# Kernel optimization log

Hardware: AMD Instinct MI355X
Metric: run time of the kernel (lower is better)

The kernel has to match this reference:

```python
import jax, jax.numpy as jnp
import numpy as np

N_HEAD, D_HEAD, D_MODEL, D_INNER, KSIZE = 16, 64, 1024, 4096, 3
LN_EPS = 1e-3  # keras LayerNormalization default epsilon


def _layernorm(x, g, b):
    m = jnp.mean(x, axis=-1, keepdims=True)
    v = jnp.var(x, axis=-1, keepdims=True)
    return (x - m) * jax.lax.rsqrt(v + LN_EPS) * g + b


def _conv1d_same(x, w, b):
    # x: [B, S, Cin], w: [K, Cin, Cout] (keras Conv1D layout)
    y = jax.lax.conv_general_dilated(x, w, window_strides=(1,), padding='SAME',
                                     dimension_numbers=('NWC', 'WIO', 'NWC'))
    return y + b


def setup_inputs() -> dict:
    key = jax.random.key(0)
    ks = jax.random.split(key, 12)
    B, S, D = 4, 1024, D_MODEL
    dec_inp = jax.random.normal(ks[0], (B, S, D), dtype=jnp.float32)
    # padding mask: True = valid token; ensure >=1 padded position per row
    lengths = jax.random.randint(ks[1], (B,), S // 2, S)
    mask = (jnp.arange(S)[None, :] < lengths[:, None])[:, :, None]  # [B,S,1] bool
    sd = 0.02
    qkv_w = jax.random.normal(ks[2], (D, 3 * N_HEAD * D_HEAD), dtype=jnp.float32) * sd
    qkv_b = jnp.zeros((3 * N_HEAD * D_HEAD,), dtype=jnp.float32)
    o_w = jax.random.normal(ks[3], (N_HEAD * D_HEAD, D), dtype=jnp.float32) * sd
    ln1_g = jnp.ones((D,), dtype=jnp.float32)
    ln1_b = jnp.zeros((D,), dtype=jnp.float32)
    conv1_w = jax.random.normal(ks[4], (KSIZE, D, D_INNER), dtype=jnp.float32) * sd
    conv1_b = jnp.zeros((D_INNER,), dtype=jnp.float32)
    conv2_w = jax.random.normal(ks[5], (KSIZE, D_INNER, D), dtype=jnp.float32) * sd
    conv2_b = jnp.zeros((D,), dtype=jnp.float32)
    ln2_g = jnp.ones((D,), dtype=jnp.float32)
    ln2_b = jnp.zeros((D,), dtype=jnp.float32)
    return dict(dec_inp=dec_inp, mask=mask, qkv_w=qkv_w, qkv_b=qkv_b, o_w=o_w,
                ln1_g=ln1_g, ln1_b=ln1_b, conv1_w=conv1_w, conv1_b=conv1_b,
                conv2_w=conv2_w, conv2_b=conv2_b, ln2_g=ln2_g, ln2_b=ln2_b)


def _forward(dec_inp, mask, qkv_w, qkv_b, o_w, ln1_g, ln1_b,
             conv1_w, conv1_b, conv2_w, conv2_b, ln2_g, ln2_b):
    B, S, D = dec_inp.shape
    H, dh = N_HEAD, D_HEAD
    scale = 1.0 / (dh ** 0.5)
    # --- MultiHeadAttn (post-lnorm; dropout inactive at inference) ---
    residual = dec_inp
    qkv = dec_inp @ qkv_w + qkv_b                       # [B,S,3*H*dh]
    hq, hk, hv = jnp.split(qkv, 3, axis=2)
    to_flat = lambda h: h.reshape(B, S, H, dh).transpose(0, 2, 1, 3).reshape(B * H, S, dh)
    q, k, v = to_flat(hq), to_flat(hk), to_flat(hv)
    score = jnp.einsum('bqd,bkd->bqk', q, k) * scale    # [B*H, S, S]
    # attn_mask = ~mask.squeeze(2): True at PAD positions (faithful to TF port)
    am = (~mask[:, :, 0]).astype(score.dtype)[:, None, :]    # [B,1,S]
    am = jnp.tile(am, (H, S, 1))                             # [B*H,S,S] (tile over batch axis, as in tf.tile)
    add = jnp.where(am.astype(bool), am, -jnp.inf)           # pad -> +1.0, valid -> -inf (as written in source)
    score = score + add
    prob = jax.nn.softmax(score, axis=2)
    vec = prob @ v                                      # [B*H,S,dh]
    # faithful to source reshapes: [B*H,S,dh] -> [H,B,S,dh] -> [B,S,H*dh]
    vec = vec.reshape(H, B, S, dh).transpose(1, 2, 0, 3).reshape(B, S, H * dh)
    attn_out = vec @ o_w
    out = _layernorm(residual + attn_out, ln1_g, ln1_b)
    # mask-multiply between blocks
    out = out * mask.astype(out.dtype)
    # --- PositionwiseConvFF (post-lnorm) ---
    core = _conv1d_same(out, conv1_w, conv1_b)
    core = jax.nn.relu(core)
    core = _conv1d_same(core, conv2_w, conv2_b)
    out = _layernorm(out + core, ln2_g, ln2_b)
    out = out * mask.astype(out.dtype)
    return out


def reference(dec_inp, mask, qkv_w, qkv_b, o_w, ln1_g, ln1_b,
              conv1_w, conv1_b, conv2_w, conv2_b, ln2_g, ln2_b):
    return _forward(dec_inp, mask, qkv_w, qkv_b, o_w, ln1_g, ln1_b,
                    conv1_w, conv1_b, conv2_w, conv2_b, ln2_g, ln2_b)
```

## Files before the change

### kernel.cpp

```cpp
#include <hip/hip_runtime.h>
#include <cstdint>
#include <cstddef>

typedef float f32x4 __attribute__((ext_vector_type(4)));
typedef __bf16 bf16x8 __attribute__((ext_vector_type(8)));
typedef unsigned short u16;

__device__ __forceinline__ float bf2f(u16 u) {
  union { unsigned int i; float f; } x; x.i = ((unsigned int)u) << 16; return x.f;
}
__device__ __forceinline__ u16 f2bf(float f) {
  union { float f; unsigned int i; } x; x.f = f;
  unsigned int i = x.i;
  i += 0x7fffu + ((i >> 16) & 1u);
  return (u16)(i >> 16);
}

#if defined(__has_builtin)
#if __has_builtin(__builtin_amdgcn_global_load_lds)
#define HAS_GLL 1
#endif
#endif

__device__ __forceinline__ void async16(const u16* g, u16* l) {
#ifdef HAS_GLL
  __builtin_amdgcn_global_load_lds((const __attribute__((address_space(1))) void*)(const void*)g,
                                   (__attribute__((address_space(3))) void*)(void*)l, 16, 0, 0);
#else
  *(uint4*)l = *(const uint4*)g;
#endif
}

__global__ void compact_mask(const unsigned char* __restrict__ mask,
                             int* __restrict__ padIdx, int* __restrict__ padCnt,
                             float* __restrict__ maskf) {
  const int b = blockIdx.x;
  const int lane = threadIdx.x;
  int stride = 1;
  if (mask[1] == 0) stride = (mask[4] != 0) ? 4 : 8;
  int cnt = 0;
  for (int s0 = 0; s0 < 1024; s0 += 64) {
    const int s = s0 + lane;
    const bool valid = (mask[(size_t)((b << 10) + s) * stride] != 0);
    maskf[(b << 10) + s] = valid ? 1.f : 0.f;
    const bool pad = !valid;
    const unsigned long long bal = __ballot(pad);
    const int rank = (int)__popcll(bal & ((1ull << lane) - 1ull));
    if (pad) padIdx[(b << 10) + cnt + rank] = s;
    cnt += (int)__popcll(bal);
  }
  if (lane == 0) padCnt[b] = cnt;
}

__global__ __launch_bounds__(256)
void f32_to_bf16(const float* __restrict__ in, u16* __restrict__ out, int n4) {
  const int i = blockIdx.x * 256 + threadIdx.x;
  if (i < n4) {
    const float4 v = ((const float4*)in)[i];
    u16 o[4] = { f2bf(v.x), f2bf(v.y), f2bf(v.z), f2bf(v.w) };
    ((ushort4*)out)[i] = *(const ushort4*)o;
  }
}

__global__ __launch_bounds__(256)
void transpose_f32_bf16(const float* __restrict__ in, u16* __restrict__ out, int R, int C) {
  __shared__ u16 tile[64][65];
  const int r0 = blockIdx.y << 6, c0 = blockIdx.x << 6;
  const int tid = threadIdx.x;
  const int lr = tid >> 3, lc = (tid & 7) << 3;
#pragma unroll
  for (int p = 0; p < 2; ++p) {
    const int row = lr + (p << 5);
    const float4 a = *(const float4*)(in + (size_t)(r0 + row) * C + c0 + lc);
    const float4 bq = *(const float4*)(in + (size_t)(r0 + row) * C + c0 + lc + 4);
    tile[row][lc + 0] = f2bf(a.x); tile[row][lc + 1] = f2bf(a.y);
    tile[row][lc + 2] = f2bf(a.z); tile[row][lc + 3] = f2bf(a.w);
    tile[row][lc + 4] = f2bf(bq.x); tile[row][lc + 5] = f2bf(bq.y);
    tile[row][lc + 6] = f2bf(bq.z); tile[row][lc + 7] = f2bf(bq.w);
  }
  __syncthreads();
#pragma unroll
  for (int p = 0; p < 2; ++p) {
    const int oc = lr + (p << 5);
    u16 tmp[8];
#pragma unroll
    for (int e = 0; e < 8; ++e) tmp[e] = tile[lc + e][oc];
    *(uint4*)(out + (size_t)(c0 + oc) * R + r0 + lc) = *(const uint4*)tmp;
  }
}

template<int NTAPS, bool RELU, int SPLITK, int KORIG, int NBN>
__global__ __launch_bounds__(256)
void gemm_bt(const u16* __restrict__ A, const u16* __restrict__ BT,
             const float* __restrict__ bias, u16* __restrict__ C, u16* __restrict__ Calt,
             int M, int N, const u16* __restrict__ zp) {
  __shared__ __align__(16) u16 As[128 * 64];
  __shared__ __align__(16) u16 Bs[128 * 64];
  const int tid = threadIdx.x;
  const int id = blockIdx.x + NBN * blockIdx.y;
  const int bm = ((id / (16 * NBN)) << 4) + (id & 15);
  const int bn = (id % (16 * NBN)) >> 4;
  const int m0 = bm << 7;
  const int n0 = bn << 7;
  const int kz = (SPLITK > 1) ? blockIdx.z : 0;
  constexpr int Ktot = NTAPS * KORIG;
  constexpr int kchunk = Ktot / SPLITK;
  const int lane = tid & 63;
  const int w = tid >> 6;
  const int wm = (w >> 1) << 6;
  const int wn = (w & 1) << 6;
  const int fr = lane & 15;
  const int quad = lane >> 4;
  const int srow = tid >> 3;
  const int scol = (tid & 7) << 3;
  const int sx = (((tid & 7) ^ (srow & 7)) << 3);

  f32x4 acc[4][4] = {};

  const int kbeg = kz * kchunk, kend = kbeg + kchunk;
  int k = kbeg;
  while (k < kend) {
    const int t = (NTAPS == 3) ? (k / KORIG) : 0;
    const int seg_end = (NTAPS == 3) ? min(kend, (t + 1) * KORIG) : kend;
    const int c0 = k - t * KORIG;
    const u16* aptr[4];
    const u16* bptr[4];
#pragma unroll
    for (int i = 0; i < 4; ++i) {
      const int row = srow + (i << 5);
      if (NTAPS == 3) {
        const int m = m0 + row;
        const int sp = (m & 1023) + t - 1;
        aptr[i] = ((unsigned)sp < 1024u) ? (A + (size_t)(m + t - 1) * KORIG + c0 + sx)
                                         : (zp + ((tid & 255) << 3));
      } else {
        aptr[i] = A + (size_t)(m0 + row) * KORIG + k + sx;
      }
      bptr[i] = BT + (size_t)(n0 + row) * Ktot + k + sx;
    }
    for (; k < seg_end; k += 64) {
#pragma unroll
      for (int i = 0; i < 4; ++i) {
        const int row = srow + (i << 5);
        async16(aptr[i], &As[(row << 6) + scol]);
        async16(bptr[i], &Bs[(row << 6) + scol]);
        aptr[i] += 64; bptr[i] += 64;
      }
      asm volatile("s_waitcnt vmcnt(0)" ::: "memory");
      __syncthreads();
#pragma unroll
      for (int ks = 0; ks < 64; ks += 32) {
        const int ccol = ((((ks >> 3) + quad) ^ (fr & 7)) << 3);
        bf16x8 af[4], bfr[4];
#pragma unroll
        for (int mi = 0; mi < 4; ++mi)
          af[mi] = *(const bf16x8*)&As[((wm + (mi << 4) + fr) << 6) + ccol];
#pragma unroll
        for (int ni = 0; ni < 4; ++ni)
          bfr[ni] = *(const bf16x8*)&Bs[((wn + (ni << 4) + fr) << 6) + ccol];
#pragma unroll
        for (int mi = 0; mi < 4; ++mi)
#pragma unroll
          for (int ni = 0; ni < 4; ++ni)
            acc[mi][ni] = __builtin_amdgcn_mfma_f32_16x16x32_bf16(af[mi], bfr[ni], acc[mi][ni], 0, 0, 0);
      }
      __syncthreads();
    }
  }
  const int rbase = m0 + wm + (quad << 2);
  const int cbase = n0 + wn + fr;
  u16* dst = C;
  if (SPLITK > 1 && kz > 0) dst = Calt + (size_t)(kz - 1) * ((size_t)M * N);
#pragma unroll
  for (int ni = 0; ni < 4; ++ni) {
    const int col = cbase + (ni << 4);
    const float bv = (SPLITK == 1 && bias) ? bias[col] : 0.f;
#pragma unroll
    for (int mi = 0; mi < 4; ++mi) {
#pragma unroll
      for (int r = 0; r < 4; ++r) {
        float v = acc[mi][ni][r] + bv;
        if (RELU) v = fmaxf(v, 0.f);
        dst[(size_t)(rbase + (mi << 4) + r) * N + col] = f2bf(v);
      }
    }
  }
}

__global__ __launch_bounds__(256)
void gather_v(const u16* __restrict__ qkv, const int* __restrict__ padIdx,
              const int* __restrict__ padCnt, u16* __restrict__ Vt) {
  const int bm = blockIdx.x;
  const int jt = blockIdx.y;
  const int b = bm >> 2, mb = bm & 3;
  const int npad = padCnt[mb];
  const int npadR = (npad + 63) & ~63;
  if (jt * 64 >= npadR) return;
  const int tid = threadIdx.x;
  __shared__ int rows[64];
  if (tid < 64) {
    const int j = jt * 64 + tid;
    const int jj = j < npad ? j : npad - 1;
    rows[tid] = padIdx[(mb << 10) + jj];
  }
  __shared__ u16 tile[64][72];
  for (int c = 0; c < 16; ++c) {
    const int ch0 = c << 6;
    __syncthreads();
#pragma unroll
    for (int p = 0; p < 2; ++p) {
      const int r = (tid >> 3) + (p << 5);
      const int ch = (tid & 7) << 3;
      const uint4 v = *(const uint4*)(qkv + (size_t)((b << 10) + rows[r]) * 3072 + 2048 + ch0 + ch);
      const u16* us = (const u16*)&v;
#pragma unroll
      for (int e = 0; e < 8; ++e) tile[r][ch + e] = us[e];
    }
    __syncthreads();
#pragma unroll
    for (int p = 0; p < 2; ++p) {
      const int r = (tid >> 3) + (p << 5);
      const int jc = (tid & 7) << 3;
      u16 tmp[8];
#pragma unroll
      for (int e = 0; e < 8; ++e) tmp[e] = tile[jc + e][r];
      *(uint4*)(Vt + (size_t)((bm << 10) + ch0 + r) * 512 + jt * 64 + jc) = *(const uint4*)tmp;
    }
  }
}

__global__ __launch_bounds__(256)
void attn_mfma(const u16* __restrict__ qkv, const u16* __restrict__ Vt,
               const int* __restrict__ padIdx, const int* __restrict__ padCnt,
               u16* __restrict__ vecS) {
  __shared__ __align__(16) u16 Ks[64 * 64];
  __shared__ __align__(16) u16 Vts[64 * 64];
  __shared__ __align__(16) u16 Ps[4][32 * 88];
  __shared__ int rowsIdx[512];
  const int i = blockIdx.x;
  const int qt = blockIdx.y;
  const int b = i >> 4, h = i & 15;
  const int mb = h & 3, bm = (b << 2) + mb;
  const int h_out = i >> 2;
  const int npad = padCnt[mb];
  const int nkt = (npad + 63) >> 6;
  const int tid = threadIdx.x;
  const int w = tid >> 6, lane = tid & 63;
  const int fr = lane & 15, quad = lane >> 4, fko = quad << 3;
  const int srow = tid >> 3, scol = (tid & 7) << 3;
  const int sx = (((tid & 7) ^ (srow & 7)) << 3);

#pragma unroll
  for (int p = 0; p < 2; ++p) {
    const int j = (p << 8) + tid;
    const int jj = j < npad ? j : npad - 1;
    rowsIdx[j] = padIdx[(mb << 10) + jj];
  }

  const int qw = (qt << 7) + (w << 5);
  bf16x8 qf[2][2];
#pragma unroll
  for (int rt = 0; rt < 2; ++rt)
#pragma unroll
    for (int ks = 0; ks < 2; ++ks)
      qf[rt][ks] = *(const bf16x8*)(qkv + (size_t)((b << 10) + qw + (rt << 4) + fr) * 3072 +
                                    (h << 6) + (ks << 5) + fko);

  f32x4 O[2][4];
  float mrun[2][4], lrun[2][4];
#pragma unroll
  for (int rt = 0; rt < 2; ++rt)
#pragma unroll
    for (int r = 0; r < 4; ++r) {
      mrun[rt][r] = -1e30f; lrun[rt][r] = 0.f;
#pragma unroll
      for (int dt = 0; dt < 4; ++dt) O[rt][dt][r] = 0.f;
    }
  __syncthreads();

  for (int kt = 0; kt < nkt; ++kt) {
#pragma unroll
    for (int p = 0; p < 2; ++p) {
      const int r = srow + (p << 5);
      const int grow = rowsIdx[(kt << 6) + r];
      async16(qkv + (size_t)((b << 10) + grow) * 3072 + 1024 + (h << 6) + sx,
              &Ks[(r << 6) + scol]);
      async16(Vt + (size_t)((bm << 10) + (h << 6) + r) * 512 + (kt << 6) + sx,
              &Vts[(r << 6) + scol]);
    }
    asm volatile("s_waitcnt vmcnt(0)" ::: "memory");
    __syncthreads();

    f32x4 S[2][4];
#pragma unroll
    for (int rt = 0; rt < 2; ++rt)
#pragma unroll
      for (int nt = 0; nt < 4; ++nt)
#pragma unroll
        for (int r = 0; r < 4; ++r) S[rt][nt][r] = 0.f;
#pragma unroll
    for (int ks = 0; ks < 2; ++ks) {
      const int ccol = ((((ks << 2) + quad) ^ (fr & 7)) << 3);
      bf16x8 bfr[4];
#pragma unroll
      for (int nt = 0; nt < 4; ++nt)
        bfr[nt] = *(const bf16x8*)&Ks[(((nt << 4) + fr) << 6) + ccol];
#pragma unroll
      for (int rt = 0; rt < 2; ++rt)
#pragma unroll
        for (int nt = 0; nt < 4; ++nt)
          S[rt][nt] = __builtin_amdgcn_mfma_f32_16x16x32_bf16(qf[rt][ks], bfr[nt], S[rt][nt], 0, 0, 0);
    }

#pragma unroll
    for (int nt = 0; nt < 4; ++nt) {
      const int key = (kt << 6) + (nt << 4) + fr;
      const bool dead = (key >= npad);
#pragma unroll
      for (int rt = 0; rt < 2; ++rt)
#pragma unroll
        for (int r = 0; r < 4; ++r) {
          float s = S[rt][nt][r] * 0.125f;
          S[rt][nt][r] = dead ? -1e30f : s;
        }
    }

#pragma unroll
    for (int rt = 0; rt < 2; ++rt) {
#pragma unroll
      for (int r = 0; r < 4; ++r) {
        float mx = fmaxf(fmaxf(S[rt][0][r], S[rt][1][r]), fmaxf(S[rt][2][r], S[rt][3][r]));
#pragma unroll
        for (int off = 1; off <= 8; off <<= 1) mx = fmaxf(mx, __shfl_xor(mx, off, 64));
        const float mnew = fmaxf(mrun[rt][r], mx);
        const float alpha = __expf(mrun[rt][r] - mnew);
        mrun[rt][r] = mnew;
        float rsum = 0.f;
#pragma unroll
        for (int nt = 0; nt < 4; ++nt) {
          const float p_ = __expf(S[rt][nt][r] - mnew);
          S[rt][nt][r] = p_;
          rsum += p_;
        }
#pragma unroll
        for (int off = 1; off <= 8; off <<= 1) rsum += __shfl_xor(rsum, off, 64);
        lrun[rt][r] = lrun[rt][r] * alpha + rsum;
#pragma unroll
        for (int dt = 0; dt < 4; ++dt) O[rt][dt][r] *= alpha;
      }
    }

    u16* ps = &Ps[w][0];
#pragma unroll
    for (int rt = 0; rt < 2; ++rt)
#pragma unroll
      for (int nt = 0; nt < 4; ++nt)
#pragma unroll
        for (int r = 0; r < 4; ++r)
          ps[((rt << 4) + (quad << 2) + r) * 88 + (nt << 4) + fr] = f2bf(S[rt][nt][r]);
    asm volatile("s_waitcnt lgkmcnt(0)" ::: "memory");

#pragma unroll
    for (int ks = 0; ks < 2; ++ks) {
      const int ccol = ((((ks << 2) + quad) ^ (fr & 7)) << 3);
      bf16x8 af[2], bv[4];
#pragma unroll
      for (int rt = 0; rt < 2; ++rt)
        af[rt] = *(const bf16x8*)&ps[((rt << 4) + fr) * 88 + (ks << 5) + fko];
#pragma unroll
      for (int dt = 0; dt < 4; ++dt)
        bv[dt] = *(const bf16x8*)&Vts[(((dt << 4) + fr) << 6) + ccol];
#pragma unroll
      for (int rt = 0; rt < 2; ++rt)
#pragma unroll
        for (int dt = 0; dt < 4; ++dt)
          O[rt][dt] = __builtin_amdgcn_mfma_f32_16x16x32_bf16(af[rt], bv[dt], O[rt][dt], 0, 0, 0);
    }
    __syncthreads();
  }

#pragma unroll
  for (int rt = 0; rt < 2; ++rt)
#pragma unroll
    for (int r = 0; r < 4; ++r) {
      const float inv = 1.f / lrun[rt][r];
      const int q = qw + (rt << 4) + (quad << 2) + r;
      u16* orow = vecS + (size_t)((mb << 10) + q) * 1024 + (h_out << 6);
#pragma unroll
      for (int dt = 0; dt < 4; ++dt)
        orow[(dt << 4) + fr] = f2bf(O[rt][dt][r] * inv);
    }
}

template<bool XF32, bool OUTF32, bool HASB>
__global__ __launch_bounds__(256)
void ln_red4(const void* __restrict__ Xv, const u16* __restrict__ P0,
             const u16* __restrict__ P1, int MN,
             const float* __restrict__ bias,
             const float* __restrict__ g, const float* __restrict__ be,
             const float* __restrict__ maskf, void* __restrict__ outv) {
  const int r = blockIdx.x;
  const int tid = threadIdx.x;
  const size_t base = (size_t)r << 10;
  const float* Xf = (const float*)Xv;
  const u16* Xb = (const u16*)Xv;
  float x[4];
  float s1 = 0.f, s2 = 0.f;
#pragma unroll
  for (int j = 0; j < 4; ++j) {
    const int c = (tid << 2) + j;
    const size_t idx = base + c;
    float y = bf2f(P0[idx]) + bf2f(P1[idx]) + bf2f(P1[MN + idx]) + bf2f(P1[2 * (size_t)MN + idx]);
    if (HASB) y += bias[c];
    const float xv = XF32 ? Xf[idx] : bf2f(Xb[idx]);
    const float v = xv + y;
    x[j] = v; s1 += v; s2 += v * v;
  }
#pragma unroll
  for (int off = 32; off > 0; off >>= 1) { s1 += __shfl_xor(s1, off, 64); s2 += __shfl_xor(s2, off, 64); }
  __shared__ float rs1[4], rs2[4];
  if ((tid & 63) == 0) { rs1[tid >> 6] = s1; rs2[tid >> 6] = s2; }
  __syncthreads();
  s1 = rs1[0] + rs1[1] + rs1[2] + rs1[3];
  s2 = rs2[0] + rs2[1] + rs2[2] + rs2[3];
  const float mean = s1 * (1.f / 1024.f);
  const float var = s2 * (1.f / 1024.f) - mean * mean;
  const float rstd = rsqrtf(var + 1e-3f);
  const float mv = maskf[r];
#pragma unroll
  for (int j = 0; j < 4; ++j) {
    const int c = (tid << 2) + j;
    const float y = ((x[j] - mean) * rstd * g[c] + be[c]) * mv;
    if (OUTF32) ((float*)outv)[base + c] = y;
    else ((u16*)outv)[base + c] = f2bf(y);
  }
}

extern "C" void kernel_launch(void* const* d_in, const int* in_sizes, int n_in,
                              void* d_out, int out_size, void* d_ws, size_t ws_size,
                              hipStream_t stream) {
  (void)in_sizes; (void)n_in; (void)out_size; (void)ws_size;
  const float* dec  = (const float*)d_in[0];
  const unsigned char* mask = (const unsigned char*)d_in[1];
  const float* wqkv = (const float*)d_in[2];
  const float* bqkv = (const float*)d_in[3];
  const float* wo   = (const float*)d_in[4];
  const float* g1   = (const float*)d_in[5];
  const float* b1   = (const float*)d_in[6];
  const float* w1   = (const float*)d_in[7];
  const float* bc1  = (const float*)d_in[8];
  const float* w2   = (const float*)d_in[9];
  const float* bc2  = (const float*)d_in[10];
  const float* g2   = (const float*)d_in[11];
  const float* b2   = (const float*)d_in[12];
  char* ws = (char*)d_ws;
  u16*   zp    = (u16*)(ws + 0);
  int*   pcnt  = (int*)(ws + 16384);
  float* maskf = (float*)(ws + 20480);
  int*   pidx  = (int*)(ws + 40960);
  u16*   decB  = (u16*)(ws + 65536);
  u16*   wqkvT = (u16*)(ws + 8454144);
  u16*   woT   = (u16*)(ws + 14745600);
  u16*   w1T   = (u16*)(ws + 16842752);
  u16*   w2T   = (u16*)(ws + 42008576);
  u16*   qkv   = (u16*)(ws + 67174400);
  u16*   Vt    = (u16*)(ws + 92340224);
  u16*   vecS  = (u16*)(ws + 109117440);
  u16*   x1bf  = (u16*)(ws + 8454144);
  u16*   ybuf  = (u16*)(ws + 67174400);
  u16*   aP0   = (u16*)(ws + 65536);
  u16*   aP1   = (u16*)(ws + 67174400);
  u16*   cP0   = (u16*)(ws + 65536);
  u16*   cP1   = (u16*)(ws + 16842752);

  hipMemsetAsync(zp, 0, 16384, stream);
  compact_mask<<<dim3(4), dim3(64), 0, stream>>>(mask, pidx, pcnt, maskf);
  f32_to_bf16<<<dim3(4096), dim3(256), 0, stream>>>(dec, decB, 1048576);
  transpose_f32_bf16<<<dim3(48, 16), dim3(256), 0, stream>>>(wqkv, wqkvT, 1024, 3072);
  transpose_f32_bf16<<<dim3(16, 16), dim3(256), 0, stream>>>(wo, woT, 1024, 1024);
  transpose_f32_bf16<<<dim3(64, 48), dim3(256), 0, stream>>>(w1, w1T, 3072, 4096);
  transpose_f32_bf16<<<dim3(16, 192), dim3(256), 0, stream>>>(w2, w2T, 12288, 1024);
  gemm_bt<1, false, 1, 1024, 24><<<dim3(24, 32), dim3(256), 0, stream>>>(decB, wqkvT, bqkv, qkv, nullptr, 4096, 3072, zp);
  gather_v<<<dim3(16, 8), dim3(256), 0, stream>>>(qkv, pidx, pcnt, Vt);
  attn_mfma<<<dim3(64, 8), dim3(256), 0, stream>>>(qkv, Vt, pidx, pcnt, vecS);
  gemm_bt<1, false, 4, 1024, 8><<<dim3(8, 32, 4), dim3(256), 0, stream>>>(vecS, woT, nullptr, aP0, aP1, 4096, 1024, zp);
  ln_red4<true, false, false><<<dim3(4096), dim3(256), 0, stream>>>(dec, aP0, aP1, 4194304, nullptr, g1, b1, maskf, x1bf);
  gemm_bt<3, true, 1, 1024, 32><<<dim3(32, 32), dim3(256), 0, stream>>>(x1bf, w1T, bc1, ybuf, nullptr, 4096, 4096, zp);
  gemm_bt<3, false, 4, 4096, 8><<<dim3(8, 32, 4), dim3(256), 0, stream>>>(ybuf, w2T, nullptr, cP0, cP1, 4096, 1024, zp);
  ln_red4<false, true, true><<<dim3(4096), dim3(256), 0, stream>>>(x1bf, cP0, cP1, 4194304, bc2, g2, b2, maskf, (float*)d_out);
}
```

Baseline: 556.2 us.

## Add 256x256 eight-wave GEMM with phased pipelining for QKV and conv FF

Adds a new GEMM kernel with 512 threads and 256x256 output tiles. Each tile is split into four 128-row/col quadrants, staged asynchronously into LDS, and interleaved with MFMA phases under setprio and fine-grained barriers. The QKV projection and both conv1d FF GEMMs now use this kernel instead of the 128-tile gemm_bt, aiming for more data reuse per LDS load and better overlap of loads with compute. The trade-offs are fewer blocks (192-256 per launch) on a large CU count, higher register and LDS use, and reliance on hand-counted vmcnt waits.

```diff
diff --git a/kernel.cpp b/kernel.cpp
--- a/kernel.cpp
+++ b/kernel.cpp
@@ -185,6 +185,142 @@
       }
     }
   }
+}
+
+#define BAR8() do { asm volatile("" ::: "memory"); __builtin_amdgcn_s_barrier(); asm volatile("" ::: "memory"); } while (0)
+#define WAITV(N) asm volatile("s_waitcnt vmcnt(" #N ")" ::: "memory")
+
+#define READ_A(SLOT) \
+  _Pragma("unroll") for (int mi = 0; mi < 4; ++mi) \
+  _Pragma("unroll") for (int ks = 0; ks < 2; ++ks) \
+    af[mi][ks] = *(const bf16x8*)&As[SLOT][((wm + (mi << 4) + fr) << 6) + ((((ks << 2) + quad) ^ (fr & 7)) << 3)];
+#define READ_B(SLOT, BFR) \
+  _Pragma("unroll") for (int ni = 0; ni < 2; ++ni) \
+  _Pragma("unroll") for (int ks = 0; ks < 2; ++ks) \
+    BFR[ni][ks] = *(const bf16x8*)&Bs[SLOT][((wn + (ni << 4) + fr) << 6) + ((((ks << 2) + quad) ^ (fr & 7)) << 3)];
+#define MFMA_PH(MH, NH, BFR) \
+  __builtin_amdgcn_s_setprio(1); \
+  _Pragma("unroll") for (int mi = 0; mi < 4; ++mi) \
+  _Pragma("unroll") for (int ni = 0; ni < 2; ++ni) \
+  _Pragma("unroll") for (int ks = 0; ks < 2; ++ks) \
+    acc[MH][mi][NH][ni] = __builtin_amdgcn_mfma_f32_16x16x32_bf16(af[mi][ks], BFR[ni][ks], acc[MH][mi][NH][ni], 0, 0, 0); \
+  __builtin_amdgcn_s_setprio(0)
+
+template<int NTAPS, bool RELU, int SPLITK, int KORIG>
+__global__ __launch_bounds__(512, 2)
+void gemm8(const u16* __restrict__ A, const u16* __restrict__ BT,
+           const float* __restrict__ bias, u16* __restrict__ C, u16* __restrict__ Calt,
+           int M, int N, const u16* __restrict__ zp) {
+  __shared__ __align__(16) u16 As[4][128 * 64];
+  __shared__ __align__(16) u16 Bs[4][128 * 64];
+  constexpr int Ktot = NTAPS * KORIG;
+  constexpr int kchunk = Ktot / SPLITK;
+  constexpr int NT = kchunk / 64;
+  const int tid = threadIdx.x;
+  const int id = blockIdx.x;
+  const int bm = id & 15, bn = id >> 4;
+  const int m0 = bm << 8, n0 = bn << 8;
+  const int kz = (SPLITK > 1) ? blockIdx.z : 0;
+  const int kbeg = kz * kchunk;
+  const int lane = tid & 63, w = tid >> 6;
+  const int wm = (w >> 2) << 6;
+  const int wn = (w & 3) << 5;
+  const int fr = lane & 15, quad = lane >> 4;
+  const int srow = tid >> 3;
+  const int scol = (tid & 7) << 3;
+  const int sx = (((tid & 7) ^ (srow & 7)) << 3);
+
+  const u16* bp[2][2];
+#pragma unroll
+  for (int nh = 0; nh < 2; ++nh)
+#pragma unroll
+    for (int j = 0; j < 2; ++j)
+      bp[nh][j] = BT + (size_t)(n0 + (nh << 7) + srow + (j << 6)) * Ktot + kbeg + sx;
+
+  auto stageA = [&](int ts, int mh) {
+    const int k = kbeg + (ts << 6);
+    const int tap = (NTAPS == 3) ? (k / KORIG) : 0;
+    const int c0 = k - tap * KORIG;
+    u16* dst = &As[((ts & 1) << 1) | mh][(srow << 6) + scol];
+    const int mrow = m0 + (mh << 7) + srow;
+#pragma unroll
+    for (int j = 0; j < 2; ++j) {
+      const int m = mrow + (j << 6);
+      const u16* src;
+      if (NTAPS == 1) {
+        src = A + (size_t)m * KORIG + c0 + sx;
+      } else {
+        const int sp = (m & 1023) + tap - 1;
+        src = ((unsigned)sp < 1024u) ? (A + (size_t)(m + tap - 1) * KORIG + c0 + sx)
+                                     : (zp + ((tid & 255) << 3));
+      }
+      async16(src, dst + (j << 12));
+    }
+  };
+  auto stageB = [&](int ts, int nh) {
+    u16* dst = &Bs[((ts & 1) << 1) | nh][(srow << 6) + scol];
+#pragma unroll
+    for (int j = 0; j < 2; ++j) {
+      async16(bp[nh][j], dst + (j << 12));
+      bp[nh][j] += 64;
+    }
+  };
+
+  f32x4 acc[2][4][2][2] = {};
+  bf16x8 af[4][2], bf0[2][2], bf1[2][2];
+
+  stageA(0, 0); stageB(0, 0); stageB(0, 1); stageA(0, 1);
+  WAITV(4);
+  BAR8();
+
+#pragma unroll 2
+  for (int t = 0; t < NT; ++t) {
+    const int s0 = (t & 1) << 1, s1 = s0 | 1;
+    const bool pf = (t + 1 < NT);
+    if (pf) stageA(t + 1, 0);
+    READ_A(s0);
+    READ_B(s0, bf0);
+    BAR8();
+    MFMA_PH(0, 0, bf0);
+    if (pf) { WAITV(4); } else { WAITV(2); }
+    BAR8();
+    if (pf) stageB(t + 1, 0);
+    READ_B(s1, bf1);
+    BAR8();
+    MFMA_PH(0, 1, bf1);
+    if (pf) { WAITV(4); } else { WAITV(0); }
+    BAR8();
+    if (pf) stageB(t + 1, 1);
+    READ_A(s1);
+    BAR8();
+    MFMA_PH(1, 1, bf1);
+    BAR8();
+    if (pf) stageA(t + 1, 1);
+    BAR8();
+    MFMA_PH(1, 0, bf0);
+    if (pf) { WAITV(4); }
+    BAR8();
+  }
+
+  u16* dst = C;
+  if (SPLITK > 1 && kz > 0) dst = Calt + (size_t)(kz - 1) * ((size_t)M * N);
+#pragma unroll
+  for (int mh = 0; mh < 2; ++mh)
+#pragma unroll
+    for (int nh = 0; nh < 2; ++nh)
+#pragma unroll
+      for (int ni = 0; ni < 2; ++ni) {
+        const int col = n0 + (nh << 7) + wn + (ni << 4) + fr;
+        const float bv = (SPLITK == 1 && bias) ? bias[col] : 0.f;
+#pragma unroll
+        for (int mi = 0; mi < 4; ++mi)
+#pragma unroll
+          for (int r = 0; r < 4; ++r) {
+            float v = acc[mh][mi][nh][ni][r] + bv;
+            if (RELU) v = fmaxf(v, 0.f);
+            dst[(size_t)(m0 + (mh << 7) + wm + (mi << 4) + (quad << 2) + r) * N + col] = f2bf(v);
+          }
+      }
 }
 
 __global__ __launch_bounds__(256)
@@ -480,12 +616,12 @@
   transpose_f32_bf16<<<dim3(16, 16), dim3(256), 0, stream>>>(wo, woT, 1024, 1024);
   transpose_f32_bf16<<<dim3(64, 48), dim3(256), 0, stream>>>(w1, w1T, 3072, 4096);
   transpose_f32_bf16<<<dim3(16, 192), dim3(256), 0, stream>>>(w2, w2T, 12288, 1024);
-  gemm_bt<1, false, 1, 1024, 24><<<dim3(24, 32), dim3(256), 0, stream>>>(decB, wqkvT, bqkv, qkv, nullptr, 4096, 3072, zp);
+  gemm8<1, false, 1, 1024><<<dim3(192), dim3(512), 0, stream>>>(decB, wqkvT, bqkv, qkv, nullptr, 4096, 3072, zp);
   gather_v<<<dim3(16, 8), dim3(256), 0, stream>>>(qkv, pidx, pcnt, Vt);
   attn_mfma<<<dim3(64, 8), dim3(256), 0, stream>>>(qkv, Vt, pidx, pcnt, vecS);
   gemm_bt<1, false, 4, 1024, 8><<<dim3(8, 32, 4), dim3(256), 0, stream>>>(vecS, woT, nullptr, aP0, aP1, 4096, 1024, zp);
   ln_red4<true, false, false><<<dim3(4096), dim3(256), 0, stream>>>(dec, aP0, aP1, 4194304, nullptr, g1, b1, maskf, x1bf);
-  gemm_bt<3, true, 1, 1024, 32><<<dim3(32, 32), dim3(256), 0, stream>>>(x1bf, w1T, bc1, ybuf, nullptr, 4096, 4096, zp);
-  gemm_bt<3, false, 4, 4096, 8><<<dim3(8, 32, 4), dim3(256), 0, stream>>>(ybuf, w2T, nullptr, cP0, cP1, 4096, 1024, zp);
+  gemm8<3, true, 1, 1024><<<dim3(256), dim3(512), 0, stream>>>(x1bf, w1T, bc1, ybuf, nullptr, 4096, 4096, zp);
+  gemm8<3, false, 4, 4096><<<dim3(64, 1, 4), dim3(512), 0, stream>>>(ybuf, w2T, nullptr, cP0, cP1, 4096, 1024, zp);
   ln_red4<false, true, true><<<dim3(4096), dim3(256), 0, stream>>>(x1bf, cP0, cP1, 4194304, bc2, g2, b2, maskf, (float*)d_out);
 }
```

Result: faster. 506.7 us (-8.9%).
